# Optimization experiments

Measured on AMD Instinct MI355X. Metric: run time of the kernel, lower is better.

Reference implementation:

```python
import jax, jax.numpy as jnp
import numpy as np

ALPHA = 0.8   # dice-score exponent
BETA = 0.2    # class-prob exponent
EPS = 1e-4    # dice denominator epsilon (SparseInst dice_score)


def _hungarian_max(cost):
    """Rectangular linear_sum_assignment(maximize=True) for a numpy (n,m) cost.
    Pads to square, runs the O(s^3) Hungarian algorithm with potentials.
    Returns (rows, cols) of length min(n,m), rows sorted (matches scipy)."""
    n, m = cost.shape
    s = max(n, m)
    c = np.zeros((s, s), dtype=np.float64)
    c[:n, :m] = -cost  # maximize -> minimize
    INF = 1e18
    u = np.zeros(s + 1)
    v = np.zeros(s + 1)
    p = np.zeros(s + 1, dtype=np.int64)
    way = np.zeros(s + 1, dtype=np.int64)
    for i in range(1, s + 1):
        p[0] = i
        j0 = 0
        minv = np.full(s + 1, INF)
        used = np.zeros(s + 1, dtype=bool)
        while True:
            used[j0] = True
            i0 = p[j0]
            cur = c[i0 - 1, :] - u[i0] - v[1:]
            free = ~used[1:]
            upd = free & (cur < minv[1:])
            minv[1:][upd] = cur[upd]
            way[1:][upd] = j0
            cand = np.where(free, minv[1:], INF)
            j1 = int(np.argmin(cand)) + 1
            delta = cand[j1 - 1]
            u[p[used]] += delta
            v[used] -= delta
            minv[~used] -= delta
            j0 = j1
            if p[j0] == 0:
                break
        while j0:
            j1 = way[j0]
            p[j0] = p[j1]
            j0 = j1
    rows, cols = [], []
    for j in range(1, s + 1):
        i = p[j]
        if i - 1 < n and j - 1 < m:
            rows.append(i - 1)
            cols.append(j - 1)
    order = np.argsort(np.asarray(rows))
    return np.asarray(rows)[order], np.asarray(cols)[order]


def _cost_matrix(pred_masks, pred_logits, tgt_masks, tgt_ids):
    B, N, H, W = pred_masks.shape
    T = tgt_masks.shape[0]
    pm = jax.nn.sigmoid(pred_masks.astype(jnp.float32)).reshape(B * N, H * W)
    # bilinear resize (align_corners=False / half-pixel) of GT masks to pred grid
    tm = jax.image.resize(tgt_masks.astype(jnp.float32), (T, H, W), method='linear')
    tm = tm.reshape(T, H * W)
    # dice score: 2<p,t> / (|p|^2 + |t|^2 + eps)   -> (B*N, T)
    num = 2.0 * jnp.einsum('qd,td->qt', pm, tm)
    den = jnp.sum(pm * pm, axis=-1)[:, None] + jnp.sum(tm * tm, axis=-1)[None, :]
    dice = num / (den + EPS)
    prob = jax.nn.sigmoid(pred_logits.astype(jnp.float32)).reshape(B * N, -1)[:, tgt_ids]
    C = dice ** ALPHA * prob ** BETA
    return C.reshape(B, N, T)


_cost_matrix_jit = jax.jit(_cost_matrix)


def setup_inputs() -> dict:
    key = jax.random.key(0)
    k1, k2, k3, k4 = jax.random.split(key, 4)
    B, N, H, W = 16, 100, 128, 128
    T, NC = 320, 80
    return {
        'pred_masks': jax.random.normal(k1, (B, N, H, W), dtype=jnp.float32),
        'pred_logits': jax.random.normal(k2, (B, N, NC), dtype=jnp.float32),
        'tgt_masks': jax.random.uniform(k3, (T, 2 * H, 2 * W), dtype=jnp.float32),
        'tgt_ids': jax.random.randint(k4, (T,), 0, NC, dtype=jnp.int64) if jax.config.jax_enable_x64 else jax.random.randint(k4, (T,), 0, NC, dtype=jnp.int32),
    }


def reference(pred_masks, pred_logits, tgt_masks, tgt_ids):
    B, N = pred_masks.shape[:2]
    T = tgt_masks.shape[0]
    per_img = T // B  # uniform sizes per image (stands in for [len(v['masks'])])
    C = _cost_matrix_jit(pred_masks, pred_logits, tgt_masks, tgt_ids)
    Cn = np.asarray(jax.device_get(C))
    rows, cols = [], []
    for b in range(B):
        r, c = _hungarian_max(Cn[b, :, b * per_img:(b + 1) * per_img])
        rows.append(r)
        cols.append(c)
    rows = jnp.asarray(np.stack(rows), dtype=jnp.int32)  # (B, per_img)
    cols = jnp.asarray(np.stack(cols), dtype=jnp.int32)  # (B, per_img)
    return C, rows, cols
```

## Files before the change

kernel.cpp:

```cpp
#include <hip/hip_runtime.h>
#include <math.h>

#define NB 16
#define NP 100
#define NT 320
#define NCLS 80
#define WO 128
#define HW 16384
#define QT 1600
#define PI 20
#define KSPLIT 8
#define KSLICE 2048
#define BK 64
#define KTILES 32
#define SRC_W 256
#define BM 64
#define BN 160
#define CH 16

typedef _Float16 half4v __attribute__((ext_vector_type(4)));
typedef _Float16 half8v __attribute__((ext_vector_type(8)));
typedef float f32x4 __attribute__((ext_vector_type(4)));

#define GLOAD_LDS16(gp, lp) __builtin_amdgcn_global_load_lds(                         \
    (const __attribute__((address_space(1))) void*)(gp),                              \
    (__attribute__((address_space(3))) void*)(lp), 16, 0, 0)

__device__ __forceinline__ float sigf(float x){ return 1.0f/(1.0f+expf(-x)); }
__device__ __forceinline__ float sigfast(float x){ return 1.0f/(1.0f+__expf(-x)); }

__device__ __forceinline__ void mkw128(int i, float* w, int* ix){
  int j0 = 2*i - 1;
  ix[0]=j0; ix[1]=j0+1; ix[2]=j0+2; ix[3]=j0+3;
  w[0]=0.125f; w[1]=0.375f; w[2]=0.375f; w[3]=0.125f;
  if (i == 0){ ix[0]=0; w[0]=0.0f; w[1]=3.0f/7.0f; w[2]=3.0f/7.0f; w[3]=1.0f/7.0f; }
  if (i == 127){ ix[3]=255; w[3]=0.0f; w[0]=1.0f/7.0f; w[1]=3.0f/7.0f; w[2]=3.0f/7.0f; }
}

__global__ __launch_bounds__(256) void k_sig(const float* __restrict__ A,
                                             _Float16* __restrict__ Ah,
                                             float* __restrict__ pq){
  const int q = blockIdx.x;
  const int tid = threadIdx.x;
  const float4* src = (const float4*)(A + (size_t)q * HW);
  half4v* dst = (half4v*)(Ah + (size_t)q * HW);
  float ss = 0.f;
  #pragma unroll
  for (int i = 0; i < 16; ++i){
    float4 v = src[i*256 + tid];
    float s0 = sigfast(v.x), s1 = sigfast(v.y), s2 = sigfast(v.z), s3 = sigfast(v.w);
    ss += s0*s0 + s1*s1 + s2*s2 + s3*s3;
    half4v hh = { (_Float16)s0, (_Float16)s1, (_Float16)s2, (_Float16)s3 };
    dst[i*256 + tid] = hh;
  }
  __shared__ float wred[4];
  for (int off = 32; off; off >>= 1) ss += __shfl_xor(ss, off);
  if ((tid & 63) == 0) wred[tid >> 6] = ss;
  __syncthreads();
  if (tid == 0) pq[q] = wred[0] + wred[1] + wred[2] + wred[3];
}

__global__ __launch_bounds__(256) void k_downsample(const float* __restrict__ tgt,
                                                    _Float16* __restrict__ tm,
                                                    float* __restrict__ tqpart){
  const int blk = blockIdx.x;
  const int t = blk >> 3;
  const int c = blk & 7;
  const int x = threadIdx.x;
  const int oy0 = c * CH;
  const int r0 = 2*oy0 - 1;
  const float* src = tgt + (size_t)t * (SRC_W*SRC_W);
  __shared__ float vbuf[CH][SRC_W];
  __shared__ float wred[4];

  float cc[34];
  #pragma unroll
  for (int li = 0; li < 34; ++li){
    int r = r0 + li; r = r < 0 ? 0 : (r > 255 ? 255 : r);
    cc[li] = src[r*SRC_W + x];
  }
  #pragma unroll
  for (int dy = 0; dy < CH; ++dy){
    int oy = oy0 + dy;
    float w0=0.125f, w1=0.375f, w2=0.375f, w3=0.125f;
    if (oy == 0){ w0=0.0f; w1=3.0f/7.0f; w2=3.0f/7.0f; w3=1.0f/7.0f; }
    if (oy == 127){ w3=0.0f; w0=1.0f/7.0f; w1=3.0f/7.0f; w2=3.0f/7.0f; }
    vbuf[dy][x] = w0*cc[2*dy] + w1*cc[2*dy+1] + w2*cc[2*dy+2] + w3*cc[2*dy+3];
  }
  __syncthreads();

  float ssq = 0.f;
  _Float16* dst = tm + (size_t)t * HW + (size_t)oy0 * WO;
  #pragma unroll
  for (int i = 0; i < 8; ++i){
    int e = x + 256*i;
    int oy = e >> 7;
    int ox = e & 127;
    float w[4]; int ix[4];
    mkw128(ox, w, ix);
    float val = w[0]*vbuf[oy][ix[0]] + w[1]*vbuf[oy][ix[1]]
              + w[2]*vbuf[oy][ix[2]] + w[3]*vbuf[oy][ix[3]];
    dst[oy*WO + ox] = (_Float16)val;
    ssq += val*val;
  }
  for (int off=32; off; off>>=1) ssq += __shfl_xor(ssq, off);
  if ((x & 63) == 0) wred[x >> 6] = ssq;
  __syncthreads();
  if (x == 0) tqpart[c*NT + t] = wred[0]+wred[1]+wred[2]+wred[3];
}

__global__ __launch_bounds__(512, 4) void k_gemm(const _Float16* __restrict__ Ah,
                                                 const _Float16* __restrict__ Bm,
                                                 float* __restrict__ part){
  __shared__ _Float16 As[2][BM*BK];
  __shared__ _Float16 Bs[2][BN*BK];
  const int tid = threadIdx.x;
  const int lane = tid & 63;
  const int wid = tid >> 6;
  const int rg = wid >> 1;
  const int cg = wid & 1;
  const int q0 = blockIdx.x * BM;
  const int t0 = blockIdx.y * BN;
  const int z  = blockIdx.z;
  const int ks = z * KSLICE;

  const int arow = tid >> 3, aslot = tid & 7;
  const _Float16* agp = Ah + (size_t)(q0 + arow)*HW + ks + ((aslot ^ (arow & 7)) * 8);

  f32x4 acc[5];
  #pragma unroll
  for (int n = 0; n < 5; ++n) acc[n] = (f32x4){0.f,0.f,0.f,0.f};

  GLOAD_LDS16(agp, &As[0][(size_t)tid*8]);
  #pragma unroll
  for (int i = 0; i < 3; ++i){
    int g = i*512 + tid;
    if (g < 1280){
      int row = g >> 3, s = g & 7;
      GLOAD_LDS16(Bm + (size_t)(t0 + row)*HW + ks + ((s ^ (row & 7)) * 8),
                  &Bs[0][(size_t)g*8]);
    }
  }
  asm volatile("s_waitcnt vmcnt(0)" ::: "memory");
  __builtin_amdgcn_s_barrier();

  for (int kt = 0; kt < KTILES; ++kt){
    const int cur = kt & 1, nxt = cur ^ 1;
    if (kt + 1 < KTILES){
      GLOAD_LDS16(agp + (kt+1)*BK, &As[nxt][(size_t)tid*8]);
      #pragma unroll
      for (int i = 0; i < 3; ++i){
        int g = i*512 + tid;
        if (g < 1280){
          int row = g >> 3, s = g & 7;
          GLOAD_LDS16(Bm + (size_t)(t0 + row)*HW + ks + (kt+1)*BK + ((s ^ (row & 7)) * 8),
                      &Bs[nxt][(size_t)g*8]);
        }
      }
    }
    #pragma unroll
    for (int s = 0; s < 2; ++s){
      half8v af, bf[5];
      {
        int r = rg*16 + (lane & 15);
        int c = s*4 + (lane >> 4);
        af = *(const half8v*)&As[cur][r*BK + ((c ^ (r & 7)) * 8)];
      }
      #pragma unroll
      for (int n = 0; n < 5; ++n){
        int r = cg*80 + n*16 + (lane & 15);
        int c = s*4 + (lane >> 4);
        bf[n] = *(const half8v*)&Bs[cur][r*BK + ((c ^ (r & 7)) * 8)];
      }
      #pragma unroll
      for (int n = 0; n < 5; ++n)
        acc[n] = __builtin_amdgcn_mfma_f32_16x16x32_f16(af, bf[n], acc[n], 0, 0, 0);
    }
    asm volatile("s_waitcnt vmcnt(0)" ::: "memory");
    __builtin_amdgcn_s_barrier();
  }

  float* op = part + (size_t)z * (QT*NT);
  {
    int qb = q0 + rg*16 + (lane >> 4)*4;
    #pragma unroll
    for (int n = 0; n < 5; ++n){
      int t = t0 + cg*80 + n*16 + (lane & 15);
      #pragma unroll
      for (int r = 0; r < 4; ++r)
        op[(size_t)(qb + r)*NT + t] = acc[n][r];
    }
  }
}

__global__ __launch_bounds__(256) void k_cost(const float* __restrict__ part,
                                              const float* __restrict__ pq,
                                              const float* __restrict__ tqpart,
                                              const float* __restrict__ logits,
                                              const int* __restrict__ ids,
                                              float* __restrict__ Cout){
  int idx = blockIdx.x * 256 + threadIdx.x;
  int q = idx / NT;
  int t = idx - q * NT;
  float num = 0.f;
  #pragma unroll
  for (int s = 0; s < KSPLIT; ++s) num += part[(size_t)s * (QT*NT) + idx];
  num *= 2.0f;
  float tqv = 0.f;
  #pragma unroll
  for (int s = 0; s < 8; ++s) tqv += tqpart[s * NT + t];
  float den = pq[q] + tqv + 1e-4f;
  float dice = num / den;
  float prob = sigf(logits[q * NCLS + ids[t]]);
  Cout[idx] = powf(dice, 0.8f) * powf(prob, 0.2f);
}

__global__ __launch_bounds__(64) void k_hung(const float* __restrict__ C,
                                             float* __restrict__ rows_out,
                                             float* __restrict__ cols_out){
  const int b = blockIdx.x;
  const int lane = threadIdx.x;
  __shared__ float negC[PI*NP];
  __shared__ double u[PI+1];
  __shared__ int p[NP+1];
  __shared__ int way[NP+1];
  for (int e = lane; e < PI*NP; e += 64){
    int i = e / NP, j = e - i*NP;
    negC[e] = -C[(size_t)(b*NP + j)*NT + (b*PI + i)];
  }
  if (lane <= PI) u[lane] = 0.0;
  for (int j = lane; j <= NP; j += 64){ p[j] = 0; way[j] = 0; }
  __syncthreads();
  const int jA = lane + 1;
  const int jB = lane + 65;
  const bool hasB = (jB <= NP);
  double vA = 0.0, vB = 0.0;
  const double INFD = 1e18;
  for (int i = 1; i <= PI; ++i){
    if (lane == 0) p[0] = i;
    __syncthreads();
    double mvA = INFD, mvB = INFD;
    bool usA = false, usB = false;
    int j0 = 0;
    int jbrk = 0;
    while (true){
      if (jA == j0) usA = true;
      if (hasB && jB == j0) usB = true;
      int i0 = p[j0];
      double ui0 = u[i0];
      double candA = INFD, candB = INFD;
      if (!usA){
        double cur = (double)negC[(i0-1)*NP + (jA-1)] - ui0 - vA;
        if (cur < mvA){ mvA = cur; way[jA] = j0; }
        candA = mvA;
      }
      if (hasB && !usB){
        double cur = (double)negC[(i0-1)*NP + (jB-1)] - ui0 - vB;
        if (cur < mvB){ mvB = cur; way[jB] = j0; }
        candB = mvB;
      }
      double bv; int bj;
      if (candB < candA){ bv = candB; bj = jB; } else { bv = candA; bj = jA; }
      for (int off = 32; off; off >>= 1){
        double ov = __shfl_xor(bv, off);
        int oj = __shfl_xor(bj, off);
        if (ov < bv || (ov == bv && oj < bj)){ bv = ov; bj = oj; }
      }
      const double delta = bv;
      if (usA){ int pj = p[jA]; u[pj] += delta; vA -= delta; }
      else mvA -= delta;
      if (hasB){
        if (usB){ int pj = p[jB]; u[pj] += delta; vB -= delta; }
        else mvB -= delta;
      }
      if (lane == 0) u[p[0]] += delta;
      __syncthreads();
      j0 = bj;
      if (p[j0] == 0){ jbrk = j0; break; }
    }
    __syncthreads();
    if (lane == 0){
      int j0a = jbrk;
      while (j0a){
        int jp = way[j0a];
        p[j0a] = p[jp];
        j0a = jp;
      }
    }
    __syncthreads();
  }
  if (lane == 0){
    int cnt = 0;
    for (int j = 1; j <= NP; ++j){
      int pi = p[j];
      if (pi != 0){
        rows_out[b*PI + cnt] = (float)(j - 1);
        cols_out[b*PI + cnt] = (float)(pi - 1);
        ++cnt;
      }
    }
  }
}

extern "C" void kernel_launch(void* const* d_in, const int* in_sizes, int n_in,
                              void* d_out, int out_size, void* d_ws, size_t ws_size,
                              hipStream_t stream){
  const float* pred_masks  = (const float*)d_in[0];
  const float* pred_logits = (const float*)d_in[1];
  const float* tgt_masks   = (const float*)d_in[2];
  const int*   tgt_ids     = (const int*)d_in[3];
  float* out = (float*)d_out;
  char* ws = (char*)d_ws;
  _Float16* Th  = (_Float16*)ws;
  size_t off = (size_t)NT*HW*2;
  float* tqpart = (float*)(ws + off);            off += 16384;
  float* pq     = (float*)(ws + off);            off += 16384;
  _Float16* Ah  = (_Float16*)(ws + off);         off += (size_t)QT*HW*2;
  float* part   = (float*)(ws + off);

  k_sig<<<QT, 256, 0, stream>>>(pred_masks, Ah, pq);
  k_downsample<<<NT*8, 256, 0, stream>>>(tgt_masks, Th, tqpart);
  dim3 g(QT/BM, NT/BN, KSPLIT);
  k_gemm<<<g, 512, 0, stream>>>(Ah, Th, part);
  k_cost<<<(QT*NT)/256, 256, 0, stream>>>(part, pq, tqpart, pred_logits, tgt_ids, out);
  k_hung<<<NB, 64, 0, stream>>>(out, out + (size_t)QT*NT, out + (size_t)QT*NT + NT);
}
```

Baseline: 127.1 us.

## Load A fragments directly to registers and triple-buffer B tiles in LDS

The GEMM kernel stops staging the A (prediction) tile through shared memory. Each lane now loads its MFMA A fragments straight from global memory into registers, prefetched two k-tiles ahead. The B tile moves to a three-stage LDS ring with a partial vmcnt wait, so two tiles of loads stay in flight while the current tile is computed. This cuts LDS traffic and barrier stalls, but raises register pressure and relies on a hand-picked vmcnt count that depends on load ordering.

```diff
diff --git a/kernel.cpp b/kernel.cpp
--- a/kernel.cpp
+++ b/kernel.cpp
@@ -112,8 +112,7 @@
 __global__ __launch_bounds__(512, 4) void k_gemm(const _Float16* __restrict__ Ah,
                                                  const _Float16* __restrict__ Bm,
                                                  float* __restrict__ part){
-  __shared__ _Float16 As[2][BM*BK];
-  __shared__ _Float16 Bs[2][BN*BK];
+  __shared__ _Float16 Bs[3][BN*BK];
   const int tid = threadIdx.x;
   const int lane = tid & 63;
   const int wid = tid >> 6;
@@ -124,14 +123,12 @@
   const int z  = blockIdx.z;
   const int ks = z * KSLICE;
 
-  const int arow = tid >> 3, aslot = tid & 7;
-  const _Float16* agp = Ah + (size_t)(q0 + arow)*HW + ks + ((aslot ^ (arow & 7)) * 8);
+  const _Float16* afp = Ah + (size_t)(q0 + rg*16 + (lane & 15)) * HW + ks + ((lane >> 4) * 8);
 
   f32x4 acc[5];
   #pragma unroll
   for (int n = 0; n < 5; ++n) acc[n] = (f32x4){0.f,0.f,0.f,0.f};
 
-  GLOAD_LDS16(agp, &As[0][(size_t)tid*8]);
   #pragma unroll
   for (int i = 0; i < 3; ++i){
     int g = i*512 + tid;
@@ -141,43 +138,70 @@
                   &Bs[0][(size_t)g*8]);
     }
   }
+  #pragma unroll
+  for (int i = 0; i < 3; ++i){
+    int g = i*512 + tid;
+    if (g < 1280){
+      int row = g >> 3, s = g & 7;
+      GLOAD_LDS16(Bm + (size_t)(t0 + row)*HW + ks + BK + ((s ^ (row & 7)) * 8),
+                  &Bs[1][(size_t)g*8]);
+    }
+  }
+  half8v aH0 = *(const half8v*)(afp);
+  half8v aH1 = *(const half8v*)(afp + 32);
+  half8v aC0 = *(const half8v*)(afp + BK);
+  half8v aC1 = *(const half8v*)(afp + BK + 32);
   asm volatile("s_waitcnt vmcnt(0)" ::: "memory");
   __builtin_amdgcn_s_barrier();
 
   for (int kt = 0; kt < KTILES; ++kt){
-    const int cur = kt & 1, nxt = cur ^ 1;
-    if (kt + 1 < KTILES){
-      GLOAD_LDS16(agp + (kt+1)*BK, &As[nxt][(size_t)tid*8]);
+    half8v aN0, aN1;
+    if (kt + 2 < KTILES){
+      _Float16* lds = &Bs[(kt+2)%3][0];
+      const _Float16* bbase = Bm + (size_t)(ks + (kt+2)*BK);
       #pragma unroll
       for (int i = 0; i < 3; ++i){
         int g = i*512 + tid;
         if (g < 1280){
           int row = g >> 3, s = g & 7;
-          GLOAD_LDS16(Bm + (size_t)(t0 + row)*HW + ks + (kt+1)*BK + ((s ^ (row & 7)) * 8),
-                      &Bs[nxt][(size_t)g*8]);
+          GLOAD_LDS16(bbase + (size_t)(t0 + row)*HW + ((s ^ (row & 7)) * 8),
+                      lds + (size_t)g*8);
         }
       }
-    }
-    #pragma unroll
-    for (int s = 0; s < 2; ++s){
-      half8v af, bf[5];
-      {
-        int r = rg*16 + (lane & 15);
-        int c = s*4 + (lane >> 4);
-        af = *(const half8v*)&As[cur][r*BK + ((c ^ (r & 7)) * 8)];
-      }
+      const _Float16* apn = afp + (kt+2)*BK;
+      aN0 = *(const half8v*)(apn);
+      aN1 = *(const half8v*)(apn + 32);
+    }
+    {
+      const _Float16* bb = &Bs[kt%3][0];
+      half8v bf[5];
       #pragma unroll
       for (int n = 0; n < 5; ++n){
         int r = cg*80 + n*16 + (lane & 15);
-        int c = s*4 + (lane >> 4);
-        bf[n] = *(const half8v*)&Bs[cur][r*BK + ((c ^ (r & 7)) * 8)];
+        int c = 0*4 + (lane >> 4);
+        bf[n] = *(const half8v*)&bb[r*BK + ((c ^ (r & 7)) * 8)];
       }
       #pragma unroll
       for (int n = 0; n < 5; ++n)
-        acc[n] = __builtin_amdgcn_mfma_f32_16x16x32_f16(af, bf[n], acc[n], 0, 0, 0);
-    }
-    asm volatile("s_waitcnt vmcnt(0)" ::: "memory");
+        acc[n] = __builtin_amdgcn_mfma_f32_16x16x32_f16(aH0, bf[n], acc[n], 0, 0, 0);
+      #pragma unroll
+      for (int n = 0; n < 5; ++n){
+        int r = cg*80 + n*16 + (lane & 15);
+        int c = 1*4 + (lane >> 4);
+        bf[n] = *(const half8v*)&bb[r*BK + ((c ^ (r & 7)) * 8)];
+      }
+      #pragma unroll
+      for (int n = 0; n < 5; ++n)
+        acc[n] = __builtin_amdgcn_mfma_f32_16x16x32_f16(aH1, bf[n], acc[n], 0, 0, 0);
+    }
+    if (kt + 2 < KTILES){
+      asm volatile("s_waitcnt vmcnt(5)" ::: "memory");
+    } else {
+      asm volatile("s_waitcnt vmcnt(0)" ::: "memory");
+    }
     __builtin_amdgcn_s_barrier();
+    aH0 = aC0; aH1 = aC1;
+    if (kt + 2 < KTILES){ aC0 = aN0; aC1 = aN1; }
   }
 
   float* op = part + (size_t)z * (QT*NT);
```

Result: slower. 139.2 us (+9.5%).
